# Kernel optimization log

Measured on AMD Instinct MI355X. Metric: run time of the kernel, lower is better.

## Reference

```python
import jax, jax.numpy as jnp
import numpy as np

D_MODEL = 1024
N_HEADS = 16
D_HEAD = D_MODEL // N_HEADS
LN_EPS = 1e-5


def setup_inputs() -> dict:
    key = jax.random.key(0)
    ks = jax.random.split(key, 8)
    B, T = 4, 2048
    s = 1.0 / np.sqrt(D_MODEL)
    return {
        "encoder_seq": jax.random.normal(ks[0], (B, T, D_MODEL), jnp.float32),
        "decoder_seq": jax.random.normal(ks[1], (B, T, D_MODEL), jnp.float32),
        "Wq": jax.random.normal(ks[2], (D_MODEL, D_MODEL), jnp.float32) * s,
        "bq": jnp.zeros((D_MODEL,), jnp.float32),
        "Wk": jax.random.normal(ks[3], (D_MODEL, D_MODEL), jnp.float32) * s,
        "bk": jnp.zeros((D_MODEL,), jnp.float32),
        "Wv": jax.random.normal(ks[4], (D_MODEL, D_MODEL), jnp.float32) * s,
        "bv": jnp.zeros((D_MODEL,), jnp.float32),
        "ln_gamma": jnp.ones((D_MODEL,), jnp.float32),
        "ln_beta": jnp.zeros((D_MODEL,), jnp.float32),
    }


def layer_norm(x, gamma, beta):
    mu = jnp.mean(x, axis=-1, keepdims=True)
    var = jnp.mean(jnp.square(x - mu), axis=-1, keepdims=True)
    return (x - mu) * jax.lax.rsqrt(var + LN_EPS) * gamma + beta


def reference(encoder_seq, decoder_seq, Wq, bq, Wk, bk, Wv, bv, ln_gamma, ln_beta):
    B, T_dec, _ = decoder_seq.shape
    T_enc = encoder_seq.shape[1]
    # projections (torch Linear: x @ W^T + b)
    q = (decoder_seq @ Wq.T + bq).reshape(B, T_dec, N_HEADS, D_HEAD)
    k = (encoder_seq @ Wk.T + bk).reshape(B, T_enc, N_HEADS, D_HEAD)
    v = (encoder_seq @ Wv.T + bv).reshape(B, T_enc, N_HEADS, D_HEAD)
    scale = 1.0 / np.sqrt(D_HEAD)
    # softmax-free attention: scale*(Q K^T) V == scale * Q (K^T V); avoid [T_dec,T_enc]
    kv = jnp.einsum("bthd,bthe->bhde", k, v)          # [B,H,dh,dh]
    att = jnp.einsum("bqhd,bhde->bqhe", q, kv) * scale  # [B,T_dec,H,dh]
    att = att.reshape(B, T_dec, D_MODEL)
    # dropout is identity in eval mode; residual + LayerNorm
    return layer_norm(att + decoder_seq, ln_gamma, ln_beta)
```

## Files before the change

### kernel.cpp

```cpp
#include <hip/hip_runtime.h>
#include <hip/hip_bf16.h>
#include <stdint.h>
#include <stddef.h>

typedef __attribute__((ext_vector_type(8))) __bf16 bf16x8;
typedef __attribute__((ext_vector_type(4))) float f32x4;

#define DMODEL 1024
#define HEADS  16
#define BATCH  4
#define TSEQ   2048
#define MROWS  (BATCH * TSEQ)

#define MiB (size_t)1048576
#define QB_OFF   ((size_t)0)
#define KB_OFF   (16 * MiB)
#define VB_OFF   (32 * MiB)
#define KVP_OFF  (48 * MiB)
#define WB_OFF   (64 * MiB)
#define KVT_OFF  (70 * MiB)

__global__ __launch_bounds__(256)
void conv_w(const float* __restrict__ Wq, const float* __restrict__ Wk,
            const float* __restrict__ Wv, __bf16* __restrict__ WB)
{
    const int bid = blockIdx.x;
    const int sel = bid >> 9, blk = bid & 511;
    const float* src = (sel == 0) ? Wq : (sel == 1) ? Wk : Wv;
    const int i = blk * 2048 + threadIdx.x * 8;
    f32x4 a = *(const f32x4*)(src + i);
    f32x4 b = *(const f32x4*)(src + i + 4);
    bf16x8 o;
#pragma unroll
    for (int j = 0; j < 4; ++j) { o[j] = (__bf16)a[j]; o[j + 4] = (__bf16)b[j]; }
    *(bf16x8*)&WB[(size_t)sel * (DMODEL * DMODEL) + i] = o;
}

__global__ __launch_bounds__(256)
void qkv_gemm(const float* __restrict__ dec, const float* __restrict__ enc,
              const __bf16* __restrict__ WB,
              const float* __restrict__ bq, const float* __restrict__ bk,
              const float* __restrict__ bv,
              __bf16* __restrict__ Qb, __bf16* __restrict__ Kb,
              __bf16* __restrict__ Vb)
{
    __shared__ __align__(16) __bf16 sA[2][128 * 32];
    __shared__ __align__(16) __bf16 sB[2][128 * 32];

    const int tid  = threadIdx.x;
    const int lane = tid & 63;
    const int wv   = tid >> 6;
    const int wm   = wv >> 1;
    const int wn   = wv & 1;

    const int bid  = blockIdx.x;
    const int slab = bid & 7;
    const int idx  = bid >> 3;
    const int bm   = slab * 8 + idx / 24;
    const int bx   = idx % 24;
    const int sel  = bx >> 3;
    const int bn   = bx & 7;

    const float*  A    = (sel == 0) ? dec : enc;
    const __bf16* W    = WB + (size_t)sel * (DMODEL * DMODEL);
    const float*  bias = (sel == 0) ? bq : (sel == 1) ? bk : bv;
    __bf16*       C    = (sel == 0) ? Qb : (sel == 1) ? Kb : Vb;

    const int l4 = lane & 15;
    const int g4 = lane >> 4;
    const int NT = DMODEL / 32;

    const int r0 = tid >> 2;
    const int k0 = (tid & 3) * 8;

    auto loadA = [&](int kt, f32x4 a[4]) {
#pragma unroll
        for (int p = 0; p < 2; ++p) {
            const float* src = A + (size_t)(bm * 128 + p * 64 + r0) * DMODEL + kt * 32 + k0;
            a[2 * p]     = *(const f32x4*)src;
            a[2 * p + 1] = *(const f32x4*)(src + 4);
        }
    };
    auto writeA = [&](int buf, f32x4 a[4]) {
#pragma unroll
        for (int p = 0; p < 2; ++p) {
            bf16x8 o;
#pragma unroll
            for (int j = 0; j < 4; ++j) {
                o[j]     = (__bf16)a[2 * p][j];
                o[j + 4] = (__bf16)a[2 * p + 1][j];
            }
            *(bf16x8*)&sA[buf][p * 2048 + tid * 8] = o;
        }
    };
    auto stageB = [&](int buf, int kt) {
#pragma unroll
        for (int p = 0; p < 2; ++p) {
            const int idx2 = p * 2048 + tid * 8;
            __builtin_amdgcn_global_load_lds(
                (const __attribute__((address_space(1))) void*)
                    (W + (size_t)(bn * 128 + p * 64 + r0) * DMODEL + kt * 32 + k0),
                (__attribute__((address_space(3))) void*)(&sB[buf][idx2]), 16, 0, 0);
        }
    };

    f32x4 acc[4][4] = {};

    {
        f32x4 a0[4];
        loadA(0, a0);
        stageB(0, 0);
        writeA(0, a0);
    }
    __syncthreads();

    int buf = 0;
    for (int kt = 0; kt < NT; ++kt) {
        f32x4 an[4];
        const bool more = (kt + 1 < NT);
        if (more) { loadA(kt + 1, an); stageB(buf ^ 1, kt + 1); }

        bf16x8 af[4], bfr[4];
#pragma unroll
        for (int m = 0; m < 4; ++m)
            af[m] = *(const bf16x8*)&sA[buf][(wm * 64 + m * 16 + l4) * 32 + g4 * 8];
#pragma unroll
        for (int n = 0; n < 4; ++n)
            bfr[n] = *(const bf16x8*)&sB[buf][(wn * 64 + n * 16 + l4) * 32 + g4 * 8];

#pragma unroll
        for (int m = 0; m < 4; ++m)
#pragma unroll
            for (int n = 0; n < 4; ++n)
                acc[m][n] = __builtin_amdgcn_mfma_f32_16x16x32_bf16(af[m], bfr[n], acc[m][n], 0, 0, 0);

        if (more) writeA(buf ^ 1, an);
        __syncthreads();
        buf ^= 1;
    }

    const int crow0 = bm * 128 + wm * 64 + g4 * 4;
    const int ccol0 = bn * 128 + wn * 64 + l4;
#pragma unroll
    for (int n = 0; n < 4; ++n) {
        const int cc = ccol0 + n * 16;
        const float bv2 = bias[cc];
#pragma unroll
        for (int m = 0; m < 4; ++m) {
            const int rr = crow0 + m * 16;
#pragma unroll
            for (int j = 0; j < 4; ++j)
                C[(size_t)(rr + j) * DMODEL + cc] = (__bf16)(acc[m][n][j] + bv2);
        }
    }
}

__global__ __launch_bounds__(256)
void kv_mm(const __bf16* __restrict__ Kb, const __bf16* __restrict__ Vb,
           float* __restrict__ kvp)
{
    __shared__ __align__(16) float Ks[128][64];
    __shared__ __align__(16) float Vs[128][64];

    const int tid = threadIdx.x;
    const int bh  = blockIdx.x;
    const int ch  = blockIdx.y;
    const int b   = bh >> 4, h = bh & 15;
    const int w   = tid >> 6, lane = tid & 63;
    const int dg  = (lane >> 3) * 8;
    const int eg  = (lane & 7) * 8;
    const size_t base = (size_t)b * TSEQ + (size_t)ch * 512;

    f32x4 acc[8][2] = {};

    for (int ss = 0; ss < 4; ++ss) {
        __syncthreads();
#pragma unroll
        for (int i = 0; i < 4; ++i) {
            const int e = i * 2048 + tid * 8;
            const int t = e >> 6, d = e & 63;
            bf16x8 k8 = *(const bf16x8*)&Kb[(base + ss * 128 + t) * DMODEL + h * 64 + d];
            bf16x8 v8 = *(const bf16x8*)&Vb[(base + ss * 128 + t) * DMODEL + h * 64 + d];
            f32x4 kf0, kf1, vf0, vf1;
#pragma unroll
            for (int j = 0; j < 4; ++j) {
                kf0[j] = (float)k8[j]; kf1[j] = (float)k8[j + 4];
                vf0[j] = (float)v8[j]; vf1[j] = (float)v8[j + 4];
            }
            *(f32x4*)&Ks[t][d]     = kf0;
            *(f32x4*)&Ks[t][d + 4] = kf1;
            *(f32x4*)&Vs[t][d]     = vf0;
            *(f32x4*)&Vs[t][d + 4] = vf1;
        }
        __syncthreads();

#pragma unroll 4
        for (int tt = 0; tt < 32; ++tt) {
            const int t = w * 32 + tt;
            f32x4 kd0 = *(const f32x4*)&Ks[t][dg];
            f32x4 kd1 = *(const f32x4*)&Ks[t][dg + 4];
            f32x4 ve0 = *(const f32x4*)&Vs[t][eg];
            f32x4 ve1 = *(const f32x4*)&Vs[t][eg + 4];
#pragma unroll
            for (int r = 0; r < 8; ++r) {
                const float kd = (r < 4) ? kd0[r] : kd1[r - 4];
                acc[r][0] += ve0 * kd;
                acc[r][1] += ve1 * kd;
            }
        }
    }

    float* o = kvp + ((size_t)(ch * 4 + w) * 64 + bh) * 4096 + (size_t)dg * 64 + eg;
#pragma unroll
    for (int r = 0; r < 8; ++r) {
        *(f32x4*)(o + r * 64)     = acc[r][0];
        *(f32x4*)(o + r * 64 + 4) = acc[r][1];
    }
}

__global__ __launch_bounds__(256)
void kv_reduce(const float* __restrict__ kvp, __bf16* __restrict__ kvT)
{
    const int idx = blockIdx.x * 256 + threadIdx.x;
    const int bh  = idx >> 12;
    const int rem = idx & 4095;
    const int d = rem >> 6, e = rem & 63;
    float s = 0.f;
#pragma unroll
    for (int c = 0; c < 16; ++c) s += kvp[((size_t)c * 64 + bh) * 4096 + rem];
    kvT[(size_t)bh * 4096 + e * 64 + d] = (__bf16)(s * 0.125f);
}

__global__ __launch_bounds__(256)
void att_ln(const __bf16* __restrict__ Q, const __bf16* __restrict__ kvT,
            const float* __restrict__ dec, const float* __restrict__ gamma,
            const float* __restrict__ beta, float* __restrict__ out)
{
    __shared__ __align__(16) __bf16 att_s[32][1032];

    const int tid  = threadIdx.x;
    const int lane = tid & 63;
    const int w    = tid >> 6;
    const int l4   = lane & 15, g4 = lane >> 4;
    const int t0   = blockIdx.x * 32;
    const int b    = t0 >> 11;

#pragma unroll
    for (int i = 0; i < 4; ++i) {
        const int h = w * 4 + i;
        f32x4 acc[2][4] = {};
#pragma unroll
        for (int kk = 0; kk < 2; ++kk) {
            bf16x8 a0 = *(const bf16x8*)&Q[(size_t)(t0 + l4) * DMODEL + h * 64 + kk * 32 + g4 * 8];
            bf16x8 a1 = *(const bf16x8*)&Q[(size_t)(t0 + 16 + l4) * DMODEL + h * 64 + kk * 32 + g4 * 8];
#pragma unroll
            for (int n = 0; n < 4; ++n) {
                bf16x8 bb = *(const bf16x8*)&kvT[(size_t)(b * 16 + h) * 4096 + (n * 16 + l4) * 64 + kk * 32 + g4 * 8];
                acc[0][n] = __builtin_amdgcn_mfma_f32_16x16x32_bf16(a0, bb, acc[0][n], 0, 0, 0);
                acc[1][n] = __builtin_amdgcn_mfma_f32_16x16x32_bf16(a1, bb, acc[1][n], 0, 0, 0);
            }
        }
#pragma unroll
        for (int m = 0; m < 2; ++m)
#pragma unroll
            for (int n = 0; n < 4; ++n)
#pragma unroll
                for (int j = 0; j < 4; ++j)
                    att_s[m * 16 + g4 * 4 + j][h * 64 + n * 16 + l4] = (__bf16)acc[m][n][j];
    }
    __syncthreads();

    const int r = tid >> 3, seg = tid & 7;
    const size_t grow = (size_t)t0 + r;
    float sum = 0.f, ss2 = 0.f;
#pragma unroll
    for (int i = 0; i < 16; ++i) {
        const int c0 = seg * 8 + i * 64;
        bf16x8 av = *(const bf16x8*)&att_s[r][c0];
        f32x4 d0 = *(const f32x4*)&dec[grow * DMODEL + c0];
        f32x4 d1 = *(const f32x4*)&dec[grow * DMODEL + c0 + 4];
        bf16x8 xs;
#pragma unroll
        for (int j = 0; j < 4; ++j) {
            const float x0 = (float)av[j] + d0[j];
            const float x1 = (float)av[j + 4] + d1[j];
            sum += x0 + x1; ss2 += x0 * x0 + x1 * x1;
            xs[j] = (__bf16)x0; xs[j + 4] = (__bf16)x1;
        }
        *(bf16x8*)&att_s[r][c0] = xs;
    }
    sum += __shfl_xor(sum, 1); ss2 += __shfl_xor(ss2, 1);
    sum += __shfl_xor(sum, 2); ss2 += __shfl_xor(ss2, 2);
    sum += __shfl_xor(sum, 4); ss2 += __shfl_xor(ss2, 4);
    const float mu   = sum * (1.f / 1024.f);
    const float var  = ss2 * (1.f / 1024.f) - mu * mu;
    const float rstd = rsqrtf(var + 1e-5f);

#pragma unroll
    for (int i = 0; i < 16; ++i) {
        const int c0 = seg * 8 + i * 64;
        bf16x8 xv = *(const bf16x8*)&att_s[r][c0];
        f32x4 g0 = *(const f32x4*)&gamma[c0];
        f32x4 g1 = *(const f32x4*)&gamma[c0 + 4];
        f32x4 b0 = *(const f32x4*)&beta[c0];
        f32x4 b1 = *(const f32x4*)&beta[c0 + 4];
        f32x4 y0, y1;
#pragma unroll
        for (int j = 0; j < 4; ++j) {
            y0[j] = ((float)xv[j]     - mu) * rstd * g0[j] + b0[j];
            y1[j] = ((float)xv[j + 4] - mu) * rstd * g1[j] + b1[j];
        }
        *(f32x4*)&out[grow * DMODEL + c0]     = y0;
        *(f32x4*)&out[grow * DMODEL + c0 + 4] = y1;
    }
}

extern "C" void kernel_launch(void* const* d_in, const int* in_sizes, int n_in,
                              void* d_out, int out_size, void* d_ws, size_t ws_size,
                              hipStream_t stream)
{
    const float* enc   = (const float*)d_in[0];
    const float* dec   = (const float*)d_in[1];
    const float* Wq    = (const float*)d_in[2];
    const float* bq    = (const float*)d_in[3];
    const float* Wk    = (const float*)d_in[4];
    const float* bk    = (const float*)d_in[5];
    const float* Wv    = (const float*)d_in[6];
    const float* bv    = (const float*)d_in[7];
    const float* gamma = (const float*)d_in[8];
    const float* beta  = (const float*)d_in[9];

    char* ws = (char*)d_ws;
    __bf16* Qb  = (__bf16*)(ws + QB_OFF);
    __bf16* Kb  = (__bf16*)(ws + KB_OFF);
    __bf16* Vb  = (__bf16*)(ws + VB_OFF);
    float*  kvp = (float*) (ws + KVP_OFF);
    __bf16* WB  = (__bf16*)(ws + WB_OFF);
    __bf16* kvT = (__bf16*)(ws + KVT_OFF);

    conv_w<<<1536, 256, 0, stream>>>(Wq, Wk, Wv, WB);
    qkv_gemm<<<1536, 256, 0, stream>>>(dec, enc, WB, bq, bk, bv, Qb, Kb, Vb);
    kv_mm<<<dim3(64, 4), 256, 0, stream>>>(Kb, Vb, kvp);
    kv_reduce<<<1024, 256, 0, stream>>>(kvp, kvT);
    att_ln<<<256, 256, 0, stream>>>(Qb, kvT, dec, gamma, beta, (float*)d_out);
}
```

Baseline: 143.3 us.

## Pre-convert encoder/decoder activations to bf16 and stage both GEMM operands via direct LDS loads

Adds a combined conversion kernel that casts the encoder and decoder activations to bf16 alongside the weights. The QKV GEMM then stages both A and B tiles with global_load_lds instead of loading fp32 A through registers and converting it inside the main loop. This is meant to halve the A-operand read traffic in the GEMM and remove register-staged conversion work from the pipeline, at the cost of an extra full pass over both activation tensors (read fp32, write bf16). The workspace layout is rearranged, and KVP_OFF now overlaps DEC_OFF; this looks safe only because decB is consumed before kv_mm writes kvp.

```diff
diff --git a/kernel.cpp b/kernel.cpp
--- a/kernel.cpp
+++ b/kernel.cpp
@@ -11,33 +11,49 @@
 #define BATCH  4
 #define TSEQ   2048
 #define MROWS  (BATCH * TSEQ)
+#define NE     (MROWS * DMODEL)
+#define NW     (DMODEL * DMODEL)
 
 #define MiB (size_t)1048576
 #define QB_OFF   ((size_t)0)
 #define KB_OFF   (16 * MiB)
 #define VB_OFF   (32 * MiB)
-#define KVP_OFF  (48 * MiB)
-#define WB_OFF   (64 * MiB)
-#define KVT_OFF  (70 * MiB)
-
-__global__ __launch_bounds__(256)
-void conv_w(const float* __restrict__ Wq, const float* __restrict__ Wk,
-            const float* __restrict__ Wv, __bf16* __restrict__ WB)
-{
-    const int bid = blockIdx.x;
-    const int sel = bid >> 9, blk = bid & 511;
-    const float* src = (sel == 0) ? Wq : (sel == 1) ? Wk : Wv;
-    const int i = blk * 2048 + threadIdx.x * 8;
-    f32x4 a = *(const f32x4*)(src + i);
-    f32x4 b = *(const f32x4*)(src + i + 4);
+#define ENC_OFF  (48 * MiB)
+#define DEC_OFF  (64 * MiB)
+#define KVP_OFF  (64 * MiB)
+#define WB_OFF   (80 * MiB)
+#define KVT_OFF  (86 * MiB)
+
+__global__ __launch_bounds__(256)
+void conv_all(const float* __restrict__ enc, const float* __restrict__ dec,
+              const float* __restrict__ Wq, const float* __restrict__ Wk,
+              const float* __restrict__ Wv,
+              __bf16* __restrict__ encB, __bf16* __restrict__ decB,
+              __bf16* __restrict__ WB)
+{
+    const int i = (blockIdx.x * 256 + threadIdx.x) * 8;
+    const float* src;
+    __bf16* dst;
+    int off;
+    if (i < NE)            { src = enc; dst = encB; off = i; }
+    else if (i < 2 * NE)   { src = dec; dst = decB; off = i - NE; }
+    else {
+        const int j = i - 2 * NE;
+        const int sel = j >> 20;
+        off = j & (NW - 1);
+        src = (sel == 0) ? Wq : (sel == 1) ? Wk : Wv;
+        dst = WB + (size_t)sel * NW;
+    }
+    f32x4 a = *(const f32x4*)(src + off);
+    f32x4 b = *(const f32x4*)(src + off + 4);
     bf16x8 o;
 #pragma unroll
     for (int j = 0; j < 4; ++j) { o[j] = (__bf16)a[j]; o[j + 4] = (__bf16)b[j]; }
-    *(bf16x8*)&WB[(size_t)sel * (DMODEL * DMODEL) + i] = o;
-}
-
-__global__ __launch_bounds__(256)
-void qkv_gemm(const float* __restrict__ dec, const float* __restrict__ enc,
+    *(bf16x8*)(dst + off) = o;
+}
+
+__global__ __launch_bounds__(256)
+void qkv_gemm(const __bf16* __restrict__ decB, const __bf16* __restrict__ encB,
               const __bf16* __restrict__ WB,
               const float* __restrict__ bq, const float* __restrict__ bk,
               const float* __restrict__ bv,
@@ -61,8 +77,8 @@
     const int sel  = bx >> 3;
     const int bn   = bx & 7;
 
-    const float*  A    = (sel == 0) ? dec : enc;
-    const __bf16* W    = WB + (size_t)sel * (DMODEL * DMODEL);
+    const __bf16* A    = (sel == 0) ? decB : encB;
+    const __bf16* W    = WB + (size_t)sel * NW;
     const float*  bias = (sel == 0) ? bq : (sel == 1) ? bk : bv;
     __bf16*       C    = (sel == 0) ? Qb : (sel == 1) ? Kb : Vb;
 
@@ -70,55 +86,31 @@
     const int g4 = lane >> 4;
     const int NT = DMODEL / 32;
 
-    const int r0 = tid >> 2;
-    const int k0 = (tid & 3) * 8;
-
-    auto loadA = [&](int kt, f32x4 a[4]) {
-#pragma unroll
-        for (int p = 0; p < 2; ++p) {
-            const float* src = A + (size_t)(bm * 128 + p * 64 + r0) * DMODEL + kt * 32 + k0;
-            a[2 * p]     = *(const f32x4*)src;
-            a[2 * p + 1] = *(const f32x4*)(src + 4);
+    const int s_row = lane >> 2;
+    const int s_col = (lane & 3) * 8;
+
+    auto stage = [&](int buf, int kt) {
+        const int k0 = kt * 32 + s_col;
+#pragma unroll
+        for (int c2 = 0; c2 < 2; ++c2) {
+            const int q = wv + c2 * 4;
+            const int r = q * 16 + s_row;
+            __builtin_amdgcn_global_load_lds(
+                (const __attribute__((address_space(1))) void*)(A + (size_t)(bm * 128 + r) * DMODEL + k0),
+                (__attribute__((address_space(3))) void*)(&sA[buf][q * 512]), 16, 0, 0);
+            __builtin_amdgcn_global_load_lds(
+                (const __attribute__((address_space(1))) void*)(W + (size_t)(bn * 128 + r) * DMODEL + k0),
+                (__attribute__((address_space(3))) void*)(&sB[buf][q * 512]), 16, 0, 0);
         }
     };
-    auto writeA = [&](int buf, f32x4 a[4]) {
-#pragma unroll
-        for (int p = 0; p < 2; ++p) {
-            bf16x8 o;
-#pragma unroll
-            for (int j = 0; j < 4; ++j) {
-                o[j]     = (__bf16)a[2 * p][j];
-                o[j + 4] = (__bf16)a[2 * p + 1][j];
-            }
-            *(bf16x8*)&sA[buf][p * 2048 + tid * 8] = o;
-        }
-    };
-    auto stageB = [&](int buf, int kt) {
-#pragma unroll
-        for (int p = 0; p < 2; ++p) {
-            const int idx2 = p * 2048 + tid * 8;
-            __builtin_amdgcn_global_load_lds(
-                (const __attribute__((address_space(1))) void*)
-                    (W + (size_t)(bn * 128 + p * 64 + r0) * DMODEL + kt * 32 + k0),
-                (__attribute__((address_space(3))) void*)(&sB[buf][idx2]), 16, 0, 0);
-        }
-    };
 
     f32x4 acc[4][4] = {};
 
-    {
-        f32x4 a0[4];
-        loadA(0, a0);
-        stageB(0, 0);
-        writeA(0, a0);
-    }
+    stage(0, 0);
     __syncthreads();
-
     int buf = 0;
     for (int kt = 0; kt < NT; ++kt) {
-        f32x4 an[4];
-        const bool more = (kt + 1 < NT);
-        if (more) { loadA(kt + 1, an); stageB(buf ^ 1, kt + 1); }
+        if (kt + 1 < NT) stage(buf ^ 1, kt + 1);
 
         bf16x8 af[4], bfr[4];
 #pragma unroll
@@ -134,7 +126,6 @@
             for (int n = 0; n < 4; ++n)
                 acc[m][n] = __builtin_amdgcn_mfma_f32_16x16x32_bf16(af[m], bfr[n], acc[m][n], 0, 0, 0);
 
-        if (more) writeA(buf ^ 1, an);
         __syncthreads();
         buf ^= 1;
     }
@@ -331,15 +322,17 @@
     const float* beta  = (const float*)d_in[9];
 
     char* ws = (char*)d_ws;
-    __bf16* Qb  = (__bf16*)(ws + QB_OFF);
-    __bf16* Kb  = (__bf16*)(ws + KB_OFF);
-    __bf16* Vb  = (__bf16*)(ws + VB_OFF);
-    float*  kvp = (float*) (ws + KVP_OFF);
-    __bf16* WB  = (__bf16*)(ws + WB_OFF);
-    __bf16* kvT = (__bf16*)(ws + KVT_OFF);
-
-    conv_w<<<1536, 256, 0, stream>>>(Wq, Wk, Wv, WB);
-    qkv_gemm<<<1536, 256, 0, stream>>>(dec, enc, WB, bq, bk, bv, Qb, Kb, Vb);
+    __bf16* Qb   = (__bf16*)(ws + QB_OFF);
+    __bf16* Kb   = (__bf16*)(ws + KB_OFF);
+    __bf16* Vb   = (__bf16*)(ws + VB_OFF);
+    __bf16* encB = (__bf16*)(ws + ENC_OFF);
+    __bf16* decB = (__bf16*)(ws + DEC_OFF);
+    float*  kvp  = (float*) (ws + KVP_OFF);
+    __bf16* WB   = (__bf16*)(ws + WB_OFF);
+    __bf16* kvT  = (__bf16*)(ws + KVT_OFF);
+
+    conv_all<<<9728, 256, 0, stream>>>(enc, dec, Wq, Wk, Wv, encB, decB, WB);
+    qkv_gemm<<<1536, 256, 0, stream>>>(decB, encB, WB, bq, bk, bv, Qb, Kb, Vb);
     kv_mm<<<dim3(64, 4), 256, 0, stream>>>(Kb, Vb, kvp);
     kv_reduce<<<1024, 256, 0, stream>>>(kvp, kvT);
     att_ln<<<256, 256, 0, stream>>>(Qb, kvT, dec, gamma, beta, (float*)d_out);
```

New measurement: 145.6 us. Within noise of the previous version (+1.6%).
